# Kernel tuning notes

Hardware: AMD Instinct MI355X
Metric: run time of the kernel (lower is better)

Reference implementation:

```python
import jax, jax.numpy as jnp
import numpy as np

B, T, D = 2, 2048, 1024
H, HKV, HD = 16, 4, 64  # num_heads, num_kv_heads, head_dim
EPS = 1.1920929e-07  # torch.finfo(float32).eps, nn.RMSNorm default


def _rmsnorm(x, g):
    return x * jax.lax.rsqrt(jnp.mean(x * x, axis=-1, keepdims=True) + EPS) * g


def _ternary(w):
    # ternary quantize {-1,0,+1} with straight-through estimator
    th = jnp.mean(jnp.abs(w))
    wt = jnp.sign(w) * (jnp.abs(w) > th).astype(w.dtype)
    return w + jax.lax.stop_gradient(wt - w)


def _bitlinear(x, w, g):
    return _rmsnorm(x, g) @ _ternary(w).T


def setup_inputs() -> dict:
    key = jax.random.key(0)
    ks = jax.random.split(key, 5)
    kaiming = lambda k, shape: jax.random.normal(k, shape, jnp.float32) * np.float32(np.sqrt(2.0 / shape[1]))
    return {
        "x": jax.random.normal(ks[0], (B, T, D), jnp.float32),
        "q_w": kaiming(ks[1], (D, D)),
        "q_g": jnp.ones((D,), jnp.float32),
        "k_w": kaiming(ks[2], (HKV * HD, D)),
        "k_g": jnp.ones((D,), jnp.float32),
        "v_w": kaiming(ks[3], (HKV * HD, D)),
        "o_w": kaiming(ks[4], (D, D)),
        "o_g": jnp.ones((D,), jnp.float32),
        "qk_gain": jnp.float32(5.25),
    }


def reference(x, q_w, q_g, k_w, k_g, v_w, o_w, o_g, qk_gain):
    b, t, d = x.shape
    q = _bitlinear(x, q_w, q_g).reshape(b, t, H, HD)          # [B,T,H,hd]
    k = _bitlinear(x, k_w, k_g).reshape(b, t, HKV, HD)        # [B,T,Hkv,hd]
    v = (x @ v_w.T).reshape(b, t, HKV, HD)                    # [B,T,Hkv,hd]
    rep = H // HKV
    k = jnp.repeat(k, rep, axis=2)                            # GQA expand -> [B,T,H,hd]
    v = jnp.repeat(v, rep, axis=2)
    scale = qk_gain / np.float32(np.sqrt(HD))
    attn = jnp.einsum('bqhd,bkhd->bhqk', q, k) * scale        # [B,H,T,T]
    causal = jnp.tril(jnp.ones((t, t), bool))
    attn = jnp.where(causal, attn, -jnp.inf)
    attn = jax.nn.softmax(attn, axis=-1)
    out = jnp.einsum('bhqk,bkhd->bqhd', attn, v).reshape(b, t, d)
    return _bitlinear(out, o_w, o_g)
```

## Files before the change

### kernel.cpp

```cpp
#include <hip/hip_runtime.h>
#include <hip/hip_bf16.h>
#include <cstdint>
#include <cstddef>

typedef unsigned short u16;
typedef unsigned int u32;
typedef __attribute__((ext_vector_type(8))) short short8v;
typedef __attribute__((ext_vector_type(4))) float f32x4;
typedef __attribute__((ext_vector_type(4))) u16 u16x4;
typedef __attribute__((ext_vector_type(8))) u16 u16x8;

static constexpr int Bc = 2, Tc = 2048, Dc = 1024, Hc = 16, HKVc = 4, HDc = 64;
static constexpr int Mc = Bc * Tc;
static constexpr float EPSc = 1.1920929e-07f;

static __device__ __forceinline__ u16 f2bf(float f) {
  u32 u = __builtin_bit_cast(u32, f);
  return (u16)((u + 0x7fffu + ((u >> 16) & 1u)) >> 16);
}
static __device__ __forceinline__ float bf2f(u16 b) {
  u32 u = ((u32)b) << 16;
  return __builtin_bit_cast(float, u);
}
static __device__ __forceinline__ float fast_exp2(float x) {
  float r;
  asm("v_exp_f32 %0, %1" : "=v"(r) : "v"(x));
  return r;
}
static __device__ __forceinline__ u32 cvt_pk_bf16(float lo, float hi) {
  u32 r;
  asm("v_cvt_pk_bf16_f32 %0, %1, %2" : "=v"(r) : "v"(lo), "v"(hi));
  return r;
}

__global__ __launch_bounds__(256) void np_leafsum_all(const float* __restrict__ q_w,
                                                      const float* __restrict__ k_w,
                                                      const float* __restrict__ o_w,
                                                      float* __restrict__ leaf) {
  int blk = blockIdx.x;
  const float* w;
  float* out;
  int lfbase;
  if (blk < 256)      { w = q_w; out = leaf;         lfbase = blk * 32; }
  else if (blk < 320) { w = k_w; out = leaf + 8192;  lfbase = (blk - 256) * 32; }
  else                { w = o_w; out = leaf + 10240; lfbase = (blk - 320) * 32; }
  int t = threadIdx.x;
  int lf = lfbase + (t >> 3), j = t & 7;
  const float* a = w + (size_t)lf * 128;
  float r = fabsf(a[j]);
#pragma unroll
  for (int i = 8; i < 128; i += 8) r += fabsf(a[i + j]);
  float x = r + __shfl_xor(r, 1);
  float y = x + __shfl_xor(x, 2);
  float z = y + __shfl_xor(y, 4);
  if (j == 0) out[lf] = z;
}

__global__ __launch_bounds__(256) void np_treemean3(const float* __restrict__ leaf,
                                                    float* __restrict__ th) {
  int m = blockIdx.x;
  const float* src = leaf + (m == 0 ? 0 : (m == 1 ? 8192 : 10240));
  int nle = (m == 1) ? 2048 : 8192;
  float inv_n = (m == 1) ? (1.0f / 262144.0f) : (1.0f / 1048576.0f);
  int t = threadIdx.x;
  int chunk = nle >> 8;
  float v[32];
  for (int i = 0; i < chunk; i += 4) {
    float4 f = *(const float4*)&src[t * chunk + i];
    v[i] = f.x; v[i + 1] = f.y; v[i + 2] = f.z; v[i + 3] = f.w;
  }
  for (int cnt = chunk >> 1; cnt >= 1; cnt >>= 1)
    for (int i = 0; i < cnt; ++i) v[i] = v[2 * i] + v[2 * i + 1];
  float s = v[0];
#pragma unroll
  for (int off = 1; off < 64; off <<= 1) s += __shfl_xor(s, off);
  __shared__ float red[4];
  if ((t & 63) == 0) red[t >> 6] = s;
  __syncthreads();
  if (t == 0) th[m] = ((red[0] + red[1]) + (red[2] + red[3])) * inv_n;
}

__global__ __launch_bounds__(256) void quant_split_all(const float* __restrict__ q_w,
                                                       const float* __restrict__ k_w,
                                                       const float* __restrict__ o_w,
                                                       const float* __restrict__ v_w,
                                                       const float* __restrict__ th,
                                                       u16* __restrict__ Wq,
                                                       u16* __restrict__ Wk,
                                                       u16* __restrict__ Wo,
                                                       u16* __restrict__ Vwh) {
  int i4 = blockIdx.x * 256 + threadIdx.x;
  if (i4 < 589824) {
    const float* w; u16* o; float t;
    int j;
    if (i4 < 262144)      { w = q_w; o = Wq; t = th[0]; j = i4; }
    else if (i4 < 327680) { w = k_w; o = Wk; t = th[1]; j = i4 - 262144; }
    else                  { w = o_w; o = Wo; t = th[2]; j = i4 - 327680; }
    float4 v = *(const float4*)&w[(size_t)j * 4];
    float y[4] = {v.x, v.y, v.z, v.w};
    u16x4 q;
#pragma unroll
    for (int c = 0; c < 4; ++c)
      q[c] = (y[c] > t) ? (u16)0x3F80 : ((y[c] < -t) ? (u16)0xBF80 : (u16)0);
    *(u16x4*)&o[(size_t)j * 4] = q;
  } else {
    int j = i4 - 589824;
    float4 v = *(const float4*)&v_w[(size_t)j * 4];
    float y[4] = {v.x, v.y, v.z, v.w};
    u16x4 h;
#pragma unroll
    for (int c = 0; c < 4; ++c) h[c] = f2bf(y[c]);
    *(u16x4*)&Vwh[(size_t)j * 4] = h;
  }
}

__global__ __launch_bounds__(256) void rmsnorm_split6(const float* __restrict__ X,
                                                      const float* __restrict__ g1,
                                                      const float* __restrict__ g2,
                                                      u16* __restrict__ H1, u16* __restrict__ L1,
                                                      u16* __restrict__ H2, u16* __restrict__ L2,
                                                      u16* __restrict__ HV) {
  int row = blockIdx.x;
  const float* xr = X + (size_t)row * Dc;
  int tid = threadIdx.x;
  float4 v = *(const float4*)&xr[tid * 4];
  float vv[4] = {v.x, v.y, v.z, v.w};
  if (HV != nullptr) {
    u16x4 h;
#pragma unroll
    for (int j = 0; j < 4; ++j) h[j] = f2bf(vv[j]);
    *(u16x4*)&HV[(size_t)row * Dc + tid * 4] = h;
  }
  float ss = v.x * v.x + v.y * v.y + v.z * v.z + v.w * v.w;
#pragma unroll
  for (int off = 1; off < 64; off <<= 1) ss += __shfl_xor(ss, off);
  __shared__ float red[4];
  if ((tid & 63) == 0) red[tid >> 6] = ss;
  __syncthreads();
  float tot = red[0] + red[1] + red[2] + red[3];
  float inv = 1.0f / sqrtf(tot * (1.0f / (float)Dc) + EPSc);
  {
    float4 a = *(const float4*)&g1[tid * 4];
    float ga[4] = {a.x, a.y, a.z, a.w};
    u16x4 h, l;
#pragma unroll
    for (int j = 0; j < 4; ++j) {
      float y = vv[j] * inv * ga[j];
      u16 hb = f2bf(y);
      h[j] = hb;
      l[j] = f2bf(y - bf2f(hb));
    }
    *(u16x4*)&H1[(size_t)row * Dc + tid * 4] = h;
    if (L1 != nullptr) *(u16x4*)&L1[(size_t)row * Dc + tid * 4] = l;
  }
  if (g2 != nullptr) {
    float4 a = *(const float4*)&g2[tid * 4];
    float ga[4] = {a.x, a.y, a.z, a.w};
    u16x4 h, l;
#pragma unroll
    for (int j = 0; j < 4; ++j) {
      float y = vv[j] * inv * ga[j];
      u16 hb = f2bf(y);
      h[j] = hb;
      l[j] = f2bf(y - bf2f(hb));
    }
    *(u16x4*)&H2[(size_t)row * Dc + tid * 4] = h;
    if (L2 != nullptr) *(u16x4*)&L2[(size_t)row * Dc + tid * 4] = l;
  }
}

template <bool PA, bool PB, int MODE, int MF, int NF>
__global__ __launch_bounds__(256, 1) void gemm_mfma(
    const u16* __restrict__ Ah, const u16* __restrict__ Al,
    const u16* __restrict__ Bh, const u16* __restrict__ Bl,
    int M, int N, int K,
    float* __restrict__ C, u16* __restrict__ O1, u16* __restrict__ O2) {
  constexpr int BM = MF * 32, BN = NF * 32;
  constexpr int APT = BM / 32;
  constexpr int BPT = BN / 32;
  __shared__ __align__(16) u16 AhS[BM * 64];
  __shared__ __align__(16) u16 AlS[PA ? BM * 64 : 8];
  __shared__ __align__(16) u16 BhS[BN * 64];
  __shared__ __align__(16) u16 BlS[PB ? BN * 64 : 8];
  int tid = threadIdx.x;
  int l = tid & 63, w = tid >> 6;
  int wm = (w >> 1) * (BM / 2), wn = (w & 1) * (BN / 2);
  int bm = blockIdx.y * BM, bn = blockIdx.x * BN;
  u16x8 rAh[APT], rAl[PA ? APT : 1], rBh[BPT], rBl[PB ? BPT : 1];
  f32x4 acc[MF][NF] = {};
#define LOADTILE(kb_)                                                               \
  {                                                                                 \
    _Pragma("unroll") for (int p = 0; p < APT; ++p) {                               \
      int idx = tid + p * 256;                                                      \
      int row = idx >> 3, cc = idx & 7;                                             \
      rAh[p] = *(const u16x8*)&Ah[(size_t)(bm + row) * K + (kb_) + cc * 8];         \
      if (PA) rAl[p] = *(const u16x8*)&Al[(size_t)(bm + row) * K + (kb_) + cc * 8]; \
    }                                                                               \
    _Pragma("unroll") for (int p = 0; p < BPT; ++p) {                               \
      int idx = tid + p * 256;                                                      \
      int row = idx >> 3, cc = idx & 7;                                             \
      rBh[p] = *(const u16x8*)&Bh[(size_t)(bn + row) * K + (kb_) + cc * 8];         \
      if (PB) rBl[p] = *(const u16x8*)&Bl[(size_t)(bn + row) * K + (kb_) + cc * 8]; \
    }                                                                               \
  }
  LOADTILE(0)
  for (int kb = 0; kb < K; kb += 64) {
    __syncthreads();
#pragma unroll
    for (int p = 0; p < APT; ++p) {
      int idx = tid + p * 256;
      int row = idx >> 3, cc = idx & 7;
      int off = row * 64 + ((cc * 8) ^ ((row & 7) << 3));
      *(u16x8*)&AhS[off] = rAh[p];
      if (PA) *(u16x8*)&AlS[off] = rAl[p];
    }
#pragma unroll
    for (int p = 0; p < BPT; ++p) {
      int idx = tid + p * 256;
      int row = idx >> 3, cc = idx & 7;
      int off = row * 64 + ((cc * 8) ^ ((row & 7) << 3));
      *(u16x8*)&BhS[off] = rBh[p];
      if (PB) *(u16x8*)&BlS[off] = rBl[p];
    }
    if (kb + 64 < K) LOADTILE(kb + 64)
    __syncthreads();
    __builtin_amdgcn_s_setprio(1);
#pragma unroll
    for (int sl = 0; sl < 2; ++sl) {
      short8v fa[MF], fal[MF], fb[NF], fbl[NF];
      int kof = (l >> 4) * 8 + sl * 32;
#pragma unroll
      for (int m = 0; m < MF; ++m) {
        int row = wm + m * 16 + (l & 15);
        int off = row * 64 + (kof ^ ((row & 7) << 3));
        fa[m] = *(const short8v*)&AhS[off];
        if (PA) fal[m] = *(const short8v*)&AlS[off];
      }
#pragma unroll
      for (int n = 0; n < NF; ++n) {
        int row = wn + n * 16 + (l & 15);
        int off = row * 64 + (kof ^ ((row & 7) << 3));
        fb[n] = *(const short8v*)&BhS[off];
        if (PB) fbl[n] = *(const short8v*)&BlS[off];
      }
#pragma unroll
      for (int m = 0; m < MF; ++m)
#pragma unroll
        for (int n = 0; n < NF; ++n) {
          acc[m][n] = __builtin_amdgcn_mfma_f32_16x16x32_bf16(fa[m], fb[n], acc[m][n], 0, 0, 0);
          if (PA)
            acc[m][n] = __builtin_amdgcn_mfma_f32_16x16x32_bf16(fal[m], fb[n], acc[m][n], 0, 0, 0);
          if (PB)
            acc[m][n] = __builtin_amdgcn_mfma_f32_16x16x32_bf16(fa[m], fbl[n], acc[m][n], 0, 0, 0);
        }
    }
    __builtin_amdgcn_s_setprio(0);
  }
#undef LOADTILE
#pragma unroll
  for (int m = 0; m < MF; ++m)
#pragma unroll
    for (int n = 0; n < NF; ++n)
#pragma unroll
      for (int r = 0; r < 4; ++r) {
        int grow = bm + wm + m * 16 + (l >> 4) * 4 + r;
        int gcol = bn + wn + n * 16 + (l & 15);
        float v = acc[m][n][r];
        if (MODE == 0) {
          C[(size_t)grow * N + gcol] = v;
        } else if (MODE == 1) {
          u16 hb = f2bf(v);
          O1[(size_t)grow * N + gcol] = hb;
          O2[(size_t)grow * N + gcol] = f2bf(v - bf2f(hb));
        } else {
          int k = gcol & 31;
          int gp = (gcol & ~31) | (((k >> 2) & 3) << 3) |
                   (((k >> 4) & 1) << 2) | (k & 3);
          O1[(size_t)grow * N + gp] = f2bf(v);
        }
      }
}

__global__ __launch_bounds__(256, 2) void attn_mfma9(
    const u16* __restrict__ Qh, const u16* __restrict__ Ql,
    const u16* __restrict__ Kh, const u16* __restrict__ Kl,
    const u16* __restrict__ Vt,
    const float* __restrict__ qk_gain,
    float* __restrict__ AO) {
  __shared__ __align__(16) u16 SM[24576];
  int tid = threadIdx.x;
  int w = tid >> 6, l = tid & 63;
  int h = blockIdx.x & 15, b = blockIdx.x >> 4;
  int by = blockIdx.y;
  int qt = (by < 8) ? (15 - by) : (by - 8);
  int q0 = qt * 128;
  int kvh = h >> 2;
  const float sc2 = qk_gain[0] * 0.125f * 1.44269504f;
  u16x8 pk[2], pl[2], pv[2];
#define AISSUE3(K0)                                                             \
  {                                                                             \
    _Pragma("unroll") for (int p = 0; p < 2; ++p) {                             \
      int idx = tid + p * 256;                                                  \
      int jj = idx >> 3, cc = idx & 7;                                          \
      size_t kb = ((size_t)(b * Tc + (K0) + jj)) * (HKVc * HDc) + kvh * 64 + cc * 8; \
      pk[p] = *(const u16x8*)&Kh[kb];                                           \
      pl[p] = *(const u16x8*)&Kl[kb];                                           \
      size_t vb = ((size_t)(kvh * 64 + jj)) * (size_t)Mc + b * Tc + (K0) + cc * 8; \
      pv[p] = *(const u16x8*)&Vt[vb];                                           \
    }                                                                           \
  }
#define WRITEBUF(BI)                                                            \
  {                                                                             \
    u16* bb = SM + (BI) * 12288;                                                \
    _Pragma("unroll") for (int p = 0; p < 2; ++p) {                             \
      int idx = tid + p * 256;                                                  \
      int jj = idx >> 3, cc = idx & 7;                                          \
      int sw = jj * 64 + ((cc * 8) ^ ((jj & 7) << 3));                          \
      *(u16x8*)&bb[sw] = pk[p];                                                 \
      *(u16x8*)&bb[4096 + sw] = pl[p];                                          \
      *(u16x8*)&bb[8192 + sw] = pv[p];                                          \
    }                                                                           \
  }
  short8v qb_h[4], qb_l[4];
#pragma unroll
  for (int qp = 0; qp < 2; ++qp) {
    size_t qrow = (size_t)(b * Tc + q0 + w * 32 + qp * 16 + (l & 15));
#pragma unroll
    for (int sl = 0; sl < 2; ++sl) {
      int dstart = (l >> 4) * 8 + sl * 32;
      qb_h[qp * 2 + sl] = *(const short8v*)&Qh[qrow * Dc + h * 64 + dstart];
      qb_l[qp * 2 + sl] = *(const short8v*)&Ql[qrow * Dc + h * 64 + dstart];
    }
  }
  f32x4 Oacc[8] = {{0,0,0,0},{0,0,0,0},{0,0,0,0},{0,0,0,0},
                   {0,0,0,0},{0,0,0,0},{0,0,0,0},{0,0,0,0}};
  float mrow[2] = {-3.0e38f, -3.0e38f};
  float lrow[2] = {0.f, 0.f};
  int qmax_w = q0 + w * 32 + 31;
  int nsteps = 2 * qt + 2;
  AISSUE3(0)
  WRITEBUF(0)
  AISSUE3(64)
  __syncthreads();
  for (int stp = 0; stp < nsteps; ++stp) {
    int k0 = stp * 64;
    u16* Kh_s = SM + (stp & 1) * 12288;
    u16* Kl_s = Kh_s + 4096;
    u16* Vt_s = Kh_s + 8192;
    if (stp + 1 < nsteps) WRITEBUF((stp + 1) & 1)
    if (stp + 2 < nsteps) AISSUE3((stp + 2) * 64)
    if (k0 <= qmax_w) {
      f32x4 s[8] = {{0,0,0,0},{0,0,0,0},{0,0,0,0},{0,0,0,0},
                    {0,0,0,0},{0,0,0,0},{0,0,0,0},{0,0,0,0}};
      __builtin_amdgcn_s_setprio(1);
#pragma unroll
      for (int kt = 0; kt < 4; ++kt) {
        int key = kt * 16 + (l & 15);
#pragma unroll
        for (int sl = 0; sl < 2; ++sl) {
          int dstart = ((l >> 4) * 8 + 32 * sl) ^ ((key & 7) << 3);
          short8v bh = *(const short8v*)&Kh_s[key * 64 + dstart];
          short8v bl = *(const short8v*)&Kl_s[key * 64 + dstart];
#pragma unroll
          for (int qp = 0; qp < 2; ++qp) {
            s[qp * 4 + kt] = __builtin_amdgcn_mfma_f32_16x16x32_bf16(bh, qb_h[qp * 2 + sl], s[qp * 4 + kt], 0, 0, 0);
            s[qp * 4 + kt] = __builtin_amdgcn_mfma_f32_16x16x32_bf16(bl, qb_h[qp * 2 + sl], s[qp * 4 + kt], 0, 0, 0);
            s[qp * 4 + kt] = __builtin_amdgcn_mfma_f32_16x16x32_bf16(bh, qb_l[qp * 2 + sl], s[qp * 4 + kt], 0, 0, 0);
          }
        }
      }
      __builtin_amdgcn_s_setprio(0);
      bool full = (k0 + 63) <= (q0 + w * 32);
      if (!full) {
#pragma unroll
        for (int qp = 0; qp < 2; ++qp) {
          int qg = q0 + w * 32 + qp * 16 + (l & 15);
#pragma unroll
          for (int kt = 0; kt < 4; ++kt)
#pragma unroll
            for (int r = 0; r < 4; ++r)
              if (k0 + kt * 16 + ((l >> 4) << 2) + r > qg) s[qp * 4 + kt][r] = -3.0e38f;
        }
      }
      float p[2][4][4];
#pragma unroll
      for (int qp = 0; qp < 2; ++qp) {
        float mk[4];
#pragma unroll
        for (int kt = 0; kt < 4; ++kt)
          mk[kt] = fmaxf(fmaxf(s[qp * 4 + kt][0], s[qp * 4 + kt][1]),
                         fmaxf(s[qp * 4 + kt][2], s[qp * 4 + kt][3]));
        float mx = fmaxf(fmaxf(mk[0], mk[1]), fmaxf(mk[2], mk[3]));
        mx = fmaxf(mx, __shfl_xor(mx, 16));
        mx = fmaxf(mx, __shfl_xor(mx, 32));
        float mnew = fmaxf(mrow[qp], mx);
        float msc = mnew * sc2;
        float corr = fast_exp2(__builtin_fmaf(mrow[qp], sc2, -msc));
        mrow[qp] = mnew;
        float sk[4];
#pragma unroll
        for (int kt = 0; kt < 4; ++kt) {
#pragma unroll
          for (int r = 0; r < 4; ++r)
            p[qp][kt][r] = fast_exp2(__builtin_fmaf(s[qp * 4 + kt][r], sc2, -msc));
          sk[kt] = (p[qp][kt][0] + p[qp][kt][1]) + (p[qp][kt][2] + p[qp][kt][3]);
        }
        float rs = (sk[0] + sk[1]) + (sk[2] + sk[3]);
        rs += __shfl_xor(rs, 16);
        rs += __shfl_xor(rs, 32);
        lrow[qp] = lrow[qp] * corr + rs;
#pragma unroll
        for (int dt = 0; dt < 4; ++dt) Oacc[qp * 4 + dt] *= corr;
      }
      short8v fbv[4];
#pragma unroll
      for (int qp = 0; qp < 2; ++qp)
#pragma unroll
        for (int sl = 0; sl < 2; ++sl) {
          union { u32 u[4]; short8v v; } fq;
          fq.u[0] = cvt_pk_bf16(p[qp][2 * sl][0], p[qp][2 * sl][1]);
          fq.u[1] = cvt_pk_bf16(p[qp][2 * sl][2], p[qp][2 * sl][3]);
          fq.u[2] = cvt_pk_bf16(p[qp][2 * sl + 1][0], p[qp][2 * sl + 1][1]);
          fq.u[3] = cvt_pk_bf16(p[qp][2 * sl + 1][2], p[qp][2 * sl + 1][3]);
          fbv[qp * 2 + sl] = fq.v;
        }
      __builtin_amdgcn_s_setprio(1);
#pragma unroll
      for (int dt = 0; dt < 4; ++dt) {
        int d = dt * 16 + (l & 15);
#pragma unroll
        for (int sl = 0; sl < 2; ++sl) {
          int kstart = ((l >> 4) * 8 + 32 * sl) ^ ((d & 7) << 3);
          short8v fav = *(const short8v*)&Vt_s[d * 64 + kstart];
#pragma unroll
          for (int qp = 0; qp < 2; ++qp)
            Oacc[qp * 4 + dt] = __builtin_amdgcn_mfma_f32_16x16x32_bf16(fav, fbv[qp * 2 + sl], Oacc[qp * 4 + dt], 0, 0, 0);
        }
      }
      __builtin_amdgcn_s_setprio(0);
    }
    __syncthreads();
  }
  float* Es = (float*)SM + w * (16 * 68);
#pragma unroll
  for (int qp = 0; qp < 2; ++qp) {
    float invl = 1.0f / lrow[qp];
#pragma unroll
    for (int dt = 0; dt < 4; ++dt)
#pragma unroll
      for (int r = 0; r < 4; ++r)
        Es[(l & 15) * 68 + dt * 16 + ((l >> 4) << 2) + r] = Oacc[qp * 4 + dt][r] * invl;
    size_t arow = ((size_t)(b * Tc + q0 + w * 32 + qp * 16 + (l >> 2))) * Dc + h * 64 + (l & 3) * 4;
#pragma unroll
    for (int j = 0; j < 4; ++j) {
      float4 vv = *(const float4*)&Es[(l >> 2) * 68 + (l & 3) * 4 + j * 16];
      *(float4*)&AO[arow + j * 16] = vv;
    }
  }
#undef AISSUE3
#undef WRITEBUF
}

extern "C" void kernel_launch(void* const* d_in, const int* in_sizes, int n_in,
                              void* d_out, int out_size, void* d_ws, size_t ws_size,
                              hipStream_t stream) {
  const float* x    = (const float*)d_in[0];
  const float* q_w  = (const float*)d_in[1];
  const float* q_g  = (const float*)d_in[2];
  const float* k_w  = (const float*)d_in[3];
  const float* k_g  = (const float*)d_in[4];
  const float* v_w  = (const float*)d_in[5];
  const float* o_w  = (const float*)d_in[6];
  const float* o_g  = (const float*)d_in[7];
  const float* qk_g = (const float*)d_in[8];

  char* base = (char*)d_ws;
  u16* Xqh = (u16*)(base + (0ull  << 20));
  u16* Xql = (u16*)(base + (8ull  << 20));
  u16* Xkh = (u16*)(base + (16ull << 20));
  u16* Xkl = (u16*)(base + (24ull << 20));
  u16* Xvh = (u16*)(base + (32ull << 20));
  u16* Xvl = (u16*)(base + (40ull << 20));
  u16* Kh  = (u16*)(base + (48ull << 20));
  u16* Kl  = (u16*)(base + (50ull << 20));
  u16* Vt  = (u16*)(base + (52ull << 20));
  u16* Wq  = (u16*)(base + (54ull << 20));
  u16* Wk  = (u16*)(base + (56ull << 20));
  u16* Wo  = (u16*)(base + (57ull << 20));
  u16* Vwh = (u16*)(base + (59ull << 20));
  float* leaf = (float*)(base + (61ull << 20));
  float* th   = leaf + 18432;
  float* AO  = (float*)base;
  u16* Xoh = Xkh;
  u16* Qh  = Xvh; u16* Ql  = Xvl;

  np_leafsum_all<<<576, 256, 0, stream>>>(q_w, k_w, o_w, leaf);
  np_treemean3<<<3, 256, 0, stream>>>(leaf, th);

  quant_split_all<<<2560, 256, 0, stream>>>(q_w, k_w, o_w, v_w, th, Wq, Wk, Wo, Vwh);

  rmsnorm_split6<<<Mc, 256, 0, stream>>>(x, q_g, k_g, Xqh, Xql, Xkh, Xkl, Xvh);

  gemm_mfma<false, false, 3, 2, 2><<<dim3(64, 4), 256, 0, stream>>>(
      Vwh, nullptr, Xvh, nullptr, 256, Mc, 1024, nullptr, Vt, nullptr);
  gemm_mfma<true, false, 1, 2, 4><<<dim3(8, 64), 256, 0, stream>>>(
      Xqh, Xql, Wq, nullptr, Mc, 1024, 1024, nullptr, Qh, Ql);
  gemm_mfma<true, false, 1, 2, 2><<<dim3(4, 64), 256, 0, stream>>>(
      Xkh, Xkl, Wk, nullptr, Mc, 256, 1024, nullptr, Kh, Kl);

  attn_mfma9<<<dim3(32, 16, 1), 256, 0, stream>>>(Qh, Ql, Kh, Kl, Vt, qk_g, AO);

  rmsnorm_split6<<<Mc, 256, 0, stream>>>(AO, o_g, nullptr, Xoh, nullptr, nullptr, nullptr,
                                         nullptr);
  gemm_mfma<false, false, 0, 2, 4><<<dim3(8, 64), 256, 0, stream>>>(
      Xoh, nullptr, Wo, nullptr, Mc, 1024, 1024, (float*)d_out, nullptr, nullptr);
}
```

Baseline: 149.7 us.

## Merge Q, K and V projection GEMMs into one grouped launch

Replaces the three separate projection GEMM launches with a single kernel whose blocks dispatch by index to the Q, K or V sub-problem, all using one fixed 64x128 tile. The K and V GEMMs previously used smaller 64x64 tiles and ran as separate launches with low block counts. Grouping them is meant to cut launch gaps and tail underutilisation, and to fill the GPU with 768 blocks. The workspace layout is reshuffled so that Q no longer aliases the X_v buffers, which are now read in the same launch.

```diff
diff --git a/kernel.cpp b/kernel.cpp
--- a/kernel.cpp
+++ b/kernel.cpp
@@ -169,25 +169,22 @@
   }
 }
 
-template <bool PA, bool PB, int MODE, int MF, int NF>
-__global__ __launch_bounds__(256, 1) void gemm_mfma(
+template <bool PA, int MODE>
+static __device__ __forceinline__ void gemm_body(
     const u16* __restrict__ Ah, const u16* __restrict__ Al,
-    const u16* __restrict__ Bh, const u16* __restrict__ Bl,
-    int M, int N, int K,
-    float* __restrict__ C, u16* __restrict__ O1, u16* __restrict__ O2) {
-  constexpr int BM = MF * 32, BN = NF * 32;
-  constexpr int APT = BM / 32;
-  constexpr int BPT = BN / 32;
-  __shared__ __align__(16) u16 AhS[BM * 64];
-  __shared__ __align__(16) u16 AlS[PA ? BM * 64 : 8];
-  __shared__ __align__(16) u16 BhS[BN * 64];
-  __shared__ __align__(16) u16 BlS[PB ? BN * 64 : 8];
+    const u16* __restrict__ Bh,
+    int N, int K, int bm, int bn,
+    float* __restrict__ C, u16* __restrict__ O1, u16* __restrict__ O2,
+    u16* smem) {
+  constexpr int APT = 2, BPT = 4;
+  u16* AhS = smem;
+  u16* AlS = smem + 4096;
+  u16* BhS = smem + 8192;
   int tid = threadIdx.x;
   int l = tid & 63, w = tid >> 6;
-  int wm = (w >> 1) * (BM / 2), wn = (w & 1) * (BN / 2);
-  int bm = blockIdx.y * BM, bn = blockIdx.x * BN;
-  u16x8 rAh[APT], rAl[PA ? APT : 1], rBh[BPT], rBl[PB ? BPT : 1];
-  f32x4 acc[MF][NF] = {};
+  int wm = (w >> 1) * 32, wn = (w & 1) * 64;
+  u16x8 rAh[APT], rAl[PA ? APT : 1], rBh[BPT];
+  f32x4 acc[2][4] = {};
 #define LOADTILE(kb_)                                                               \
   {                                                                                 \
     _Pragma("unroll") for (int p = 0; p < APT; ++p) {                               \
@@ -200,7 +197,6 @@
       int idx = tid + p * 256;                                                      \
       int row = idx >> 3, cc = idx & 7;                                             \
       rBh[p] = *(const u16x8*)&Bh[(size_t)(bn + row) * K + (kb_) + cc * 8];         \
-      if (PB) rBl[p] = *(const u16x8*)&Bl[(size_t)(bn + row) * K + (kb_) + cc * 8]; \
     }                                                                               \
   }
   LOADTILE(0)
@@ -220,47 +216,43 @@
       int row = idx >> 3, cc = idx & 7;
       int off = row * 64 + ((cc * 8) ^ ((row & 7) << 3));
       *(u16x8*)&BhS[off] = rBh[p];
-      if (PB) *(u16x8*)&BlS[off] = rBl[p];
     }
     if (kb + 64 < K) LOADTILE(kb + 64)
     __syncthreads();
     __builtin_amdgcn_s_setprio(1);
 #pragma unroll
     for (int sl = 0; sl < 2; ++sl) {
-      short8v fa[MF], fal[MF], fb[NF], fbl[NF];
+      short8v fa[2], fal[2], fb[4];
       int kof = (l >> 4) * 8 + sl * 32;
 #pragma unroll
-      for (int m = 0; m < MF; ++m) {
+      for (int m = 0; m < 2; ++m) {
         int row = wm + m * 16 + (l & 15);
         int off = row * 64 + (kof ^ ((row & 7) << 3));
         fa[m] = *(const short8v*)&AhS[off];
         if (PA) fal[m] = *(const short8v*)&AlS[off];
       }
 #pragma unroll
-      for (int n = 0; n < NF; ++n) {
+      for (int n = 0; n < 4; ++n) {
         int row = wn + n * 16 + (l & 15);
         int off = row * 64 + (kof ^ ((row & 7) << 3));
         fb[n] = *(const short8v*)&BhS[off];
-        if (PB) fbl[n] = *(const short8v*)&BlS[off];
-      }
-#pragma unroll
-      for (int m = 0; m < MF; ++m)
-#pragma unroll
-        for (int n = 0; n < NF; ++n) {
+      }
+#pragma unroll
+      for (int m = 0; m < 2; ++m)
+#pragma unroll
+        for (int n = 0; n < 4; ++n) {
           acc[m][n] = __builtin_amdgcn_mfma_f32_16x16x32_bf16(fa[m], fb[n], acc[m][n], 0, 0, 0);
           if (PA)
             acc[m][n] = __builtin_amdgcn_mfma_f32_16x16x32_bf16(fal[m], fb[n], acc[m][n], 0, 0, 0);
-          if (PB)
-            acc[m][n] = __builtin_amdgcn_mfma_f32_16x16x32_bf16(fa[m], fbl[n], acc[m][n], 0, 0, 0);
         }
     }
     __builtin_amdgcn_s_setprio(0);
   }
 #undef LOADTILE
 #pragma unroll
-  for (int m = 0; m < MF; ++m)
-#pragma unroll
-    for (int n = 0; n < NF; ++n)
+  for (int m = 0; m < 2; ++m)
+#pragma unroll
+    for (int n = 0; n < 4; ++n)
 #pragma unroll
       for (int r = 0; r < 4; ++r) {
         int grow = bm + wm + m * 16 + (l >> 4) * 4 + r;
@@ -279,6 +271,37 @@
           O1[(size_t)grow * N + gp] = f2bf(v);
         }
       }
+}
+
+__global__ __launch_bounds__(256, 1) void qkv_mega(
+    const u16* __restrict__ Xqh, const u16* __restrict__ Xql, const u16* __restrict__ Wq,
+    const u16* __restrict__ Xkh, const u16* __restrict__ Xkl, const u16* __restrict__ Wk,
+    const u16* __restrict__ Xvh, const u16* __restrict__ Vwh,
+    u16* __restrict__ Qh, u16* __restrict__ Ql,
+    u16* __restrict__ Kh, u16* __restrict__ Kl,
+    u16* __restrict__ Vt) {
+  __shared__ __align__(16) u16 SMEM[16384];
+  int bx = blockIdx.x;
+  if (bx < 512) {
+    int bm = (bx >> 3) * 64, bn = (bx & 7) * 128;
+    gemm_body<true, 1>(Xqh, Xql, Wq, 1024, 1024, bm, bn, nullptr, Qh, Ql, SMEM);
+  } else if (bx < 640) {
+    int t = bx - 512;
+    int bm = (t >> 1) * 64, bn = (t & 1) * 128;
+    gemm_body<true, 1>(Xkh, Xkl, Wk, 256, 1024, bm, bn, nullptr, Kh, Kl, SMEM);
+  } else {
+    int t = bx - 640;
+    int bm = (t >> 5) * 64, bn = (t & 31) * 128;
+    gemm_body<false, 3>(Vwh, nullptr, Xvh, 4096, 1024, bm, bn, nullptr, Vt, nullptr, SMEM);
+  }
+}
+
+__global__ __launch_bounds__(256, 1) void o_gemm(
+    const u16* __restrict__ Ah, const u16* __restrict__ Bh,
+    float* __restrict__ C) {
+  __shared__ __align__(16) u16 SMEM[16384];
+  int bm = blockIdx.y * 64, bn = blockIdx.x * 128;
+  gemm_body<false, 0>(Ah, nullptr, Bh, 1024, 1024, bm, bn, C, nullptr, nullptr, SMEM);
 }
 
 __global__ __launch_bounds__(256, 2) void attn_mfma9(
@@ -480,19 +503,19 @@
   u16* Xkh = (u16*)(base + (16ull << 20));
   u16* Xkl = (u16*)(base + (24ull << 20));
   u16* Xvh = (u16*)(base + (32ull << 20));
-  u16* Xvl = (u16*)(base + (40ull << 20));
-  u16* Kh  = (u16*)(base + (48ull << 20));
-  u16* Kl  = (u16*)(base + (50ull << 20));
-  u16* Vt  = (u16*)(base + (52ull << 20));
-  u16* Wq  = (u16*)(base + (54ull << 20));
-  u16* Wk  = (u16*)(base + (56ull << 20));
-  u16* Wo  = (u16*)(base + (57ull << 20));
-  u16* Vwh = (u16*)(base + (59ull << 20));
-  float* leaf = (float*)(base + (61ull << 20));
+  u16* Qh  = (u16*)(base + (40ull << 20));
+  u16* Ql  = (u16*)(base + (48ull << 20));
+  u16* Kh  = (u16*)(base + (56ull << 20));
+  u16* Kl  = (u16*)(base + (58ull << 20));
+  u16* Vt  = (u16*)(base + (60ull << 20));
+  u16* Wq  = (u16*)(base + (62ull << 20));
+  u16* Wk  = (u16*)(base + (64ull << 20));
+  u16* Wo  = (u16*)(base + (64ull << 20) + (512ull << 10));
+  u16* Vwh = (u16*)(base + (66ull << 20) + (512ull << 10));
+  float* leaf = (float*)(base + (67ull << 20));
   float* th   = leaf + 18432;
   float* AO  = (float*)base;
   u16* Xoh = Xkh;
-  u16* Qh  = Xvh; u16* Ql  = Xvl;
 
   np_leafsum_all<<<576, 256, 0, stream>>>(q_w, k_w, o_w, leaf);
   np_treemean3<<<3, 256, 0, stream>>>(leaf, th);
@@ -501,17 +524,12 @@
 
   rmsnorm_split6<<<Mc, 256, 0, stream>>>(x, q_g, k_g, Xqh, Xql, Xkh, Xkl, Xvh);
 
-  gemm_mfma<false, false, 3, 2, 2><<<dim3(64, 4), 256, 0, stream>>>(
-      Vwh, nullptr, Xvh, nullptr, 256, Mc, 1024, nullptr, Vt, nullptr);
-  gemm_mfma<true, false, 1, 2, 4><<<dim3(8, 64), 256, 0, stream>>>(
-      Xqh, Xql, Wq, nullptr, Mc, 1024, 1024, nullptr, Qh, Ql);
-  gemm_mfma<true, false, 1, 2, 2><<<dim3(4, 64), 256, 0, stream>>>(
-      Xkh, Xkl, Wk, nullptr, Mc, 256, 1024, nullptr, Kh, Kl);
+  qkv_mega<<<768, 256, 0, stream>>>(Xqh, Xql, Wq, Xkh, Xkl, Wk, Xvh, Vwh,
+                                    Qh, Ql, Kh, Kl, Vt);
 
   attn_mfma9<<<dim3(32, 16, 1), 256, 0, stream>>>(Qh, Ql, Kh, Kl, Vt, qk_g, AO);
 
   rmsnorm_split6<<<Mc, 256, 0, stream>>>(AO, o_g, nullptr, Xoh, nullptr, nullptr, nullptr,
                                          nullptr);
-  gemm_mfma<false, false, 0, 2, 4><<<dim3(8, 64), 256, 0, stream>>>(
-      Xoh, nullptr, Wo, nullptr, Mc, 1024, 1024, (float*)d_out, nullptr, nullptr);
-}
+  o_gemm<<<dim3(8, 64), 256, 0, stream>>>(Xoh, Wo, (float*)d_out);
+}
```

After: 138.7 us. -7.4%, faster.
